# Kernel optimization log

Measured on AMD Instinct MI355X. Metric: run time of the kernel, lower is better.

## Reference

```python
import jax, jax.numpy as jnp
import numpy as np

D = 64          # node_hidden_dim
MP_STEPS = 6    # num_step_message_passing
S2S_STEPS = 6   # num_step_set2set
LSTM_LAYERS = 3 # num_layer_set2set


def setup_inputs() -> dict:
    key = jax.random.key(0)
    ks = jax.random.split(key, 32)
    N, E, B = 10000, 50000, 500
    node_in, edge_in, edge_hid, out_dim = 15, 5, 128, 12
    s = 0.1
    inp = {}
    inp["node_feat"] = jax.random.normal(ks[0], (N, node_in), jnp.float32)
    inp["edge_feat"] = jax.random.normal(ks[1], (E, edge_in), jnp.float32)
    inp["src"] = jax.random.randint(ks[2], (E,), 0, N)
    inp["dst"] = jax.random.randint(ks[3], (E,), 0, N)
    inp["graph_ids"] = jnp.sort(jax.random.randint(ks[4], (N,), 0, B))
    inp["num_graphs"] = B
    # lin0
    inp["lin0_W"] = jax.random.normal(ks[5], (node_in, D), jnp.float32) * s
    inp["lin0_b"] = jnp.zeros((D,), jnp.float32)
    # edge network MLP (Linear -> ReLU -> Linear), output reshaped to D x D per edge
    inp["em_W1"] = jax.random.normal(ks[6], (edge_in, edge_hid), jnp.float32) * s
    inp["em_b1"] = jnp.zeros((edge_hid,), jnp.float32)
    inp["em_W2"] = jax.random.normal(ks[7], (edge_hid, D * D), jnp.float32) * 0.02
    inp["em_b2"] = jnp.zeros((D * D,), jnp.float32)
    inp["conv_bias"] = jnp.zeros((D,), jnp.float32)
    # GRU (input D, hidden D), torch layout: [3*D, in], gate order r,z,n
    inp["gru_Wih"] = jax.random.normal(ks[8], (3 * D, D), jnp.float32) * s
    inp["gru_Whh"] = jax.random.normal(ks[9], (3 * D, D), jnp.float32) * s
    inp["gru_bih"] = jnp.zeros((3 * D,), jnp.float32)
    inp["gru_bhh"] = jnp.zeros((3 * D,), jnp.float32)
    # Set2Set LSTM: input 2*D, hidden D, 3 layers. torch layout [4*D, in], gates i,f,g,o
    inp["lstm0_Wih"] = jax.random.normal(ks[10], (4 * D, 2 * D), jnp.float32) * s
    inp["lstm0_Whh"] = jax.random.normal(ks[11], (4 * D, D), jnp.float32) * s
    inp["lstm0_bih"] = jnp.zeros((4 * D,), jnp.float32)
    inp["lstm0_bhh"] = jnp.zeros((4 * D,), jnp.float32)
    inp["lstm12_Wih"] = jax.random.normal(ks[12], (2, 4 * D, D), jnp.float32) * s
    inp["lstm12_Whh"] = jax.random.normal(ks[13], (2, 4 * D, D), jnp.float32) * s
    inp["lstm12_bih"] = jnp.zeros((2, 4 * D), jnp.float32)
    inp["lstm12_bhh"] = jnp.zeros((2, 4 * D), jnp.float32)
    # output head
    inp["lin1_W"] = jax.random.normal(ks[14], (2 * D, D), jnp.float32) * s
    inp["lin1_b"] = jnp.zeros((D,), jnp.float32)
    inp["lin2_W"] = jax.random.normal(ks[15], (D, out_dim), jnp.float32) * s
    inp["lin2_b"] = jnp.zeros((out_dim,), jnp.float32)
    return inp


def _mpnn(node_feat, edge_feat, src, dst, graph_ids, num_graphs,
          lin0_W, lin0_b, em_W1, em_b1, em_W2, em_b2, conv_bias,
          gru_Wih, gru_Whh, gru_bih, gru_bhh,
          lstm0_Wih, lstm0_Whh, lstm0_bih, lstm0_bhh,
          lstm12_Wih, lstm12_Whh, lstm12_bih, lstm12_bhh,
          lin1_W, lin1_b, lin2_W, lin2_b):
    N = node_feat.shape[0]
    E = edge_feat.shape[0]
    B = num_graphs
    # initial node embedding
    out = jax.nn.relu(node_feat @ lin0_W + lin0_b)      # [N, D]
    h = out                                             # GRU hidden (seq_len=1, 1 layer)
    # per-edge weight matrices (edge features are static across steps)
    We = (jax.nn.relu(edge_feat @ em_W1 + em_b1) @ em_W2 + em_b2).reshape(E, D, D)
    for _ in range(MP_STEPS):
        # NNConv: gather src -> per-edge matvec -> scatter-add to dst
        msg = jnp.einsum('ei,eio->eo', out[src], We)    # [E, D]
        agg = jax.ops.segment_sum(msg, dst, num_segments=N) + conv_bias
        m = jax.nn.relu(agg)                            # [N, D]
        # GRU cell (torch gate order r, z, n)
        gx = m @ gru_Wih.T + gru_bih
        gh = h @ gru_Whh.T + gru_bhh
        rx, zx, nx = jnp.split(gx, 3, axis=-1)
        rh, zh, nh = jnp.split(gh, 3, axis=-1)
        r = jax.nn.sigmoid(rx + rh)
        z = jax.nn.sigmoid(zx + zh)
        n = jnp.tanh(nx + r * nh)
        h = (1.0 - z) * n + z * h
        out = h
    # Set2Set readout: 3-layer LSTM over steps, attention over nodes per graph
    h_l = [jnp.zeros((B, D), out.dtype) for _ in range(LSTM_LAYERS)]
    c_l = [jnp.zeros((B, D), out.dtype) for _ in range(LSTM_LAYERS)]
    q_star = jnp.zeros((B, 2 * D), out.dtype)
    for _ in range(S2S_STEPS):
        x = q_star
        for l in range(LSTM_LAYERS):
            if l == 0:
                Wih, Whh, bih, bhh = lstm0_Wih, lstm0_Whh, lstm0_bih, lstm0_bhh
            else:
                Wih, Whh = lstm12_Wih[l - 1], lstm12_Whh[l - 1]
                bih, bhh = lstm12_bih[l - 1], lstm12_bhh[l - 1]
            g = x @ Wih.T + bih + h_l[l] @ Whh.T + bhh
            i_g, f_g, g_g, o_g = jnp.split(g, 4, axis=-1)
            c_l[l] = jax.nn.sigmoid(f_g) * c_l[l] + jax.nn.sigmoid(i_g) * jnp.tanh(g_g)
            h_l[l] = jax.nn.sigmoid(o_g) * jnp.tanh(c_l[l])
            x = h_l[l]
        q = x                                           # [B, D]
        # segment softmax attention
        e = jnp.sum(out * q[graph_ids], axis=-1)        # [N]
        emax = jax.ops.segment_max(e, graph_ids, num_segments=B)
        ex = jnp.exp(e - emax[graph_ids])
        denom = jax.ops.segment_sum(ex, graph_ids, num_segments=B)
        alpha = ex / denom[graph_ids]                   # [N]
        readout = jax.ops.segment_sum(alpha[:, None] * out, graph_ids, num_segments=B)
        q_star = jnp.concatenate([q, readout], axis=-1) # [B, 2D]
    y = jax.nn.relu(q_star @ lin1_W + lin1_b) @ lin2_W + lin2_b
    return y


def reference(node_feat, edge_feat, src, dst, graph_ids, num_graphs,
              lin0_W, lin0_b, em_W1, em_b1, em_W2, em_b2, conv_bias,
              gru_Wih, gru_Whh, gru_bih, gru_bhh,
              lstm0_Wih, lstm0_Whh, lstm0_bih, lstm0_bhh,
              lstm12_Wih, lstm12_Whh, lstm12_bih, lstm12_bhh,
              lin1_W, lin1_b, lin2_W, lin2_b):
    return _mpnn(node_feat, edge_feat, src, dst, graph_ids, num_graphs,
                 lin0_W, lin0_b, em_W1, em_b1, em_W2, em_b2, conv_bias,
                 gru_Wih, gru_Whh, gru_bih, gru_bhh,
                 lstm0_Wih, lstm0_Whh, lstm0_bih, lstm0_bhh,
                 lstm12_Wih, lstm12_Whh, lstm12_bih, lstm12_bhh,
                 lin1_W, lin1_b, lin2_W, lin2_b)
```

## Files before the change

### kernel.cpp

```cpp
#include <hip/hip_runtime.h>
#include <math.h>

#define NGRAPH 500
#define MP_STEPS 6
#define S2S_STEPS 6
#define S2S_CAP 64

typedef _Float16 h8 __attribute__((ext_vector_type(8)));
typedef float f4 __attribute__((ext_vector_type(4)));

__device__ __forceinline__ float sigmoidf_(float v){ return 1.0f/(1.0f + expf(-v)); }

__global__ void k_zero(float* __restrict__ p, int n){
  int i = blockIdx.x*256 + threadIdx.x;
  if(i < n) p[i] = 0.f;
}

__global__ void k_lin0(const float* __restrict__ nf, const float* __restrict__ W,
                       const float* __restrict__ b, const float* __restrict__ B2,
                       float* __restrict__ x, float* __restrict__ bm, int N){
  int n = blockIdx.x*4 + (threadIdx.x >> 6);
  int d = threadIdx.x & 63;
  if(n >= N) return;
  float acc = b[d];
#pragma unroll
  for(int i=0;i<15;i++) acc = fmaf(nf[n*15+i], W[i*64+d], acc);
  float xv = fmaxf(acc, 0.0f);
  x[n*64+d] = xv;
  float bmv = 0.f;
  for(int k=0;k<64;k++){
    float xk = __shfl(xv, k, 64);
    bmv = fmaf(xk, B2[k*64+d], bmv);
  }
  bm[(size_t)n*64+d] = bmv;
}

__global__ void k_edgeh(const float* __restrict__ ef, const float* __restrict__ W1,
                        const float* __restrict__ b1, _Float16* __restrict__ he, int E){
  int e = blockIdx.x*2 + (threadIdx.x >> 7);
  int h = threadIdx.x & 127;
  if(e >= E) return;
  float acc = b1[h];
#pragma unroll
  for(int i=0;i<5;i++) acc = fmaf(ef[e*5+i], W1[i*128+h], acc);
  he[(size_t)e*128 + h] = (_Float16)fmaxf(acc, 0.f);
}

__global__ void k_prepW2(const float* __restrict__ W2, _Float16* __restrict__ W2T){
  int idx = blockIdx.x*256 + threadIdx.x;
  if(idx >= 4096*128) return;
  int n = idx >> 7, k = idx & 127;
  W2T[idx] = (_Float16)W2[(size_t)k*4096 + n];
}

__global__ __launch_bounds__(256, 2) void k_fmsg(
    const _Float16* __restrict__ he,
    const _Float16* __restrict__ W2T,
    const float* __restrict__ x,
    const float* __restrict__ bm,
    const int* __restrict__ src, const int* __restrict__ dst,
    float* __restrict__ agg, int E)
{
  __shared__ _Float16 hs[128*128];
  __shared__ float xsT[64*132];
  __shared__ int ds_dst[128];
  __shared__ int ds_src[128];
  const int tid  = threadIdx.x;
  const int og   = tid >> 6;
  const int lane = tid & 63;
  const int quad = lane >> 4;
  const int l15  = lane & 15;
  const int e0   = blockIdx.x * 128;

  for(int t = tid; t < 2048; t += 256){
    int r = t >> 4, c = t & 15;
    uint4 v = make_uint4(0,0,0,0);
    if(e0 + r < E) v = *(const uint4*)&he[(size_t)(e0+r)*128 + c*8];
    *(uint4*)&hs[r*128 + c*8] = v;
  }
  {
    int j = tid >> 1, half = tid & 1;
    int sj = (e0 + j < E) ? src[e0 + j] : 0;
    const float4* xr = (const float4*)(x + (size_t)sj*64) + half*8;
#pragma unroll
    for(int k=0;k<8;k++){
      float4 v = xr[k];
      int ib = half*32 + k*4;
      xsT[(ib+0)*132 + j] = v.x;
      xsT[(ib+1)*132 + j] = v.y;
      xsT[(ib+2)*132 + j] = v.z;
      xsT[(ib+3)*132 + j] = v.w;
    }
  }
  if(tid < 128){
    ds_dst[tid] = (e0 + tid < E) ? dst[e0 + tid] : 0;
    ds_src[tid] = (e0 + tid < E) ? src[e0 + tid] : 0;
  }
  __syncthreads();

  h8 af[8][4];
#pragma unroll
  for(int mt=0;mt<8;mt++)
#pragma unroll
    for(int ks=0;ks<4;ks++)
      af[mt][ks] = *(const h8*)&hs[(mt*16 + l15)*128 + ks*32 + (quad<<3)];

  const _Float16* bbase = W2T + (size_t)(og*16 + l15)*128 + (quad<<3);

  f4 macc[8];
#pragma unroll
  for(int mt=0;mt<8;mt++) macc[mt] = (f4){0.f,0.f,0.f,0.f};

#pragma unroll 1
  for(int i=0;i<64;i++){
    const _Float16* bp = bbase + (size_t)i*64*128;
    h8 bf0 = *(const h8*)(bp);
    h8 bf1 = *(const h8*)(bp + 32);
    h8 bf2 = *(const h8*)(bp + 64);
    h8 bf3 = *(const h8*)(bp + 96);
    f4 g[8];
#pragma unroll
    for(int mt=0;mt<8;mt++) g[mt] = (f4){0.f,0.f,0.f,0.f};
#pragma unroll
    for(int mt=0;mt<8;mt++) g[mt] = __builtin_amdgcn_mfma_f32_16x16x32_f16(af[mt][0], bf0, g[mt], 0,0,0);
#pragma unroll
    for(int mt=0;mt<8;mt++) g[mt] = __builtin_amdgcn_mfma_f32_16x16x32_f16(af[mt][1], bf1, g[mt], 0,0,0);
#pragma unroll
    for(int mt=0;mt<8;mt++) g[mt] = __builtin_amdgcn_mfma_f32_16x16x32_f16(af[mt][2], bf2, g[mt], 0,0,0);
#pragma unroll
    for(int mt=0;mt<8;mt++) g[mt] = __builtin_amdgcn_mfma_f32_16x16x32_f16(af[mt][3], bf3, g[mt], 0,0,0);
#pragma unroll
    for(int mt=0;mt<8;mt++){
      f4 xf = *(const f4*)&xsT[i*132 + mt*16 + (quad<<2)];
      macc[mt] += xf * g[mt];
    }
  }

  const int col = og*16 + l15;
#pragma unroll
  for(int mt=0;mt<8;mt++){
#pragma unroll
    for(int r=0;r<4;r++){
      int edge = mt*16 + (quad<<2) + r;
      if(e0 + edge < E){
        float v = macc[mt][r] + bm[(size_t)ds_src[edge]*64 + col];
        atomicAdd(&agg[(size_t)ds_dst[edge]*64 + col], v);
      }
    }
  }
}

__global__ __launch_bounds__(256) void k_gru2(
    float* __restrict__ x, float* __restrict__ agg, const float* __restrict__ cb,
    const float* __restrict__ WihT, const float* __restrict__ WhhT,
    const float* __restrict__ bih, const float* __restrict__ bhh,
    const float* __restrict__ B2, float* __restrict__ bm, int N)
{
  __shared__ float ms[32*64], hs2[32*64];
  const int tid = threadIdx.x;
  const int n0 = blockIdx.x*32;
  for(int t=tid; t<2048; t+=256){
    int n = n0 + (t>>6), d = t&63;
    float mv=0.f, hv=0.f;
    if(n < N){
      mv = fmaxf(agg[(size_t)n*64+d] + cb[d], 0.f);
      agg[(size_t)n*64+d] = 0.f;
      hv = x[(size_t)n*64+d];
    }
    ms[t]=mv; hs2[t]=hv;
  }
  __syncthreads();
  const int gx = tid & 31, ng = tid >> 5;
  float ar[4][2]={{0}}, az[4][2]={{0}}, anx[4][2]={{0}}, anh[4][2]={{0}};
#pragma unroll 4
  for(int k=0;k<64;k++){
    float wi0=WihT[k*192+gx],     wi1=WihT[k*192+gx+32];
    float wi2=WihT[k*192+gx+64],  wi3=WihT[k*192+gx+96];
    float wi4=WihT[k*192+gx+128], wi5=WihT[k*192+gx+160];
    float wh0=WhhT[k*192+gx],     wh1=WhhT[k*192+gx+32];
    float wh2=WhhT[k*192+gx+64],  wh3=WhhT[k*192+gx+96];
    float wh4=WhhT[k*192+gx+128], wh5=WhhT[k*192+gx+160];
#pragma unroll
    for(int j=0;j<4;j++){
      float mk = ms[(ng*4+j)*64+k], hk = hs2[(ng*4+j)*64+k];
      ar[j][0] = fmaf(mk,wi0, fmaf(hk,wh0, ar[j][0]));
      ar[j][1] = fmaf(mk,wi1, fmaf(hk,wh1, ar[j][1]));
      az[j][0] = fmaf(mk,wi2, fmaf(hk,wh2, az[j][0]));
      az[j][1] = fmaf(mk,wi3, fmaf(hk,wh3, az[j][1]));
      anx[j][0]= fmaf(mk,wi4, anx[j][0]);
      anx[j][1]= fmaf(mk,wi5, anx[j][1]);
      anh[j][0]= fmaf(hk,wh4, anh[j][0]);
      anh[j][1]= fmaf(hk,wh5, anh[j][1]);
    }
  }
  float xn[4][2];
#pragma unroll
  for(int j=0;j<4;j++){
#pragma unroll
    for(int c=0;c<2;c++){
      int d = gx + 32*c;
      float r  = sigmoidf_(ar[j][c] + bih[d]     + bhh[d]);
      float z  = sigmoidf_(az[j][c] + bih[64+d]  + bhh[64+d]);
      float nn = tanhf(anx[j][c] + bih[128+d] + r*(anh[j][c] + bhh[128+d]));
      float hv = hs2[(ng*4+j)*64+d];
      xn[j][c] = (1.f - z)*nn + z*hv;
    }
  }
  __syncthreads();
#pragma unroll
  for(int j=0;j<4;j++){
#pragma unroll
    for(int c=0;c<2;c++){
      int n = n0 + ng*4 + j;
      ms[(ng*4+j)*64 + gx + 32*c] = xn[j][c];
      if(n < N) x[(size_t)n*64 + gx + 32*c] = xn[j][c];
    }
  }
  __syncthreads();
  float bmv[4][2] = {{0}};
#pragma unroll 4
  for(int d=0;d<64;d++){
    float b0 = B2[d*64+gx], b1 = B2[d*64+gx+32];
#pragma unroll
    for(int j=0;j<4;j++){
      float xd = ms[(ng*4+j)*64 + d];
      bmv[j][0] = fmaf(xd, b0, bmv[j][0]);
      bmv[j][1] = fmaf(xd, b1, bmv[j][1]);
    }
  }
#pragma unroll
  for(int j=0;j<4;j++){
    int n = n0 + ng*4 + j;
    if(n < N){
      bm[(size_t)n*64 + gx]      = bmv[j][0];
      bm[(size_t)n*64 + gx + 32] = bmv[j][1];
    }
  }
}

__global__ void k_tr_gru(const float* __restrict__ Wih, const float* __restrict__ Whh,
                         float* __restrict__ WihT, float* __restrict__ WhhT){
  int idx = blockIdx.x*256 + threadIdx.x;
  if(idx < 192*64){
    int r = idx/64, i = idx%64;
    WihT[i*192 + r] = Wih[idx];
    WhhT[i*192 + r] = Whh[idx];
  }
}

__device__ __forceinline__ int lbound(const int* __restrict__ a, int n, int v){
  int lo=0, hi=n;
  while(lo<hi){ int mid=(lo+hi)>>1; if(a[mid]<v) lo=mid+1; else hi=mid; }
  return lo;
}

template<int IN>
__device__ __forceinline__ void lstm_row(
    const float* __restrict__ xin, float* __restrict__ hv, float* __restrict__ cv,
    const float* __restrict__ Wih,
    const float* __restrict__ Whh,
    const float* __restrict__ bi, const float* __restrict__ bh,
    float* __restrict__ gs, int t)
{
  const float* wr = Wih + t*IN;
  const float* hr = Whh + t*64;
  float a0=0.f,a1=0.f,a2=0.f,a3=0.f;
#pragma unroll 8
  for(int k=0;k<IN;k+=4){
    f4 w = *(const f4*)&wr[k];
    f4 xv = *(const f4*)&xin[k];
    a0 = fmaf(w[0], xv[0], a0);
    a1 = fmaf(w[1], xv[1], a1);
    a2 = fmaf(w[2], xv[2], a2);
    a3 = fmaf(w[3], xv[3], a3);
  }
#pragma unroll 8
  for(int k=0;k<64;k+=4){
    f4 w = *(const f4*)&hr[k];
    f4 hvv = *(const f4*)&hv[k];
    a0 = fmaf(w[0], hvv[0], a0);
    a1 = fmaf(w[1], hvv[1], a1);
    a2 = fmaf(w[2], hvv[2], a2);
    a3 = fmaf(w[3], hvv[3], a3);
  }
  gs[t] = (a0+a1)+(a2+a3) + bi[t] + bh[t];
  __syncthreads();
  if(t < 64){
    float ig = sigmoidf_(gs[t]);
    float fg = sigmoidf_(gs[64+t]);
    float gg = tanhf(gs[128+t]);
    float og = sigmoidf_(gs[192+t]);
    float cn = fg*cv[t] + ig*gg;
    cv[t] = cn;
    hv[t] = og*tanhf(cn);
  }
  __syncthreads();
}

__global__ __launch_bounds__(256) void k_s2s(
    const float* __restrict__ x, const int* __restrict__ gid, int N,
    const float* __restrict__ l0_Wih, const float* __restrict__ l0_Whh,
    const float* __restrict__ l0_bih, const float* __restrict__ l0_bhh,
    const float* __restrict__ l12_Wih, const float* __restrict__ l12_Whh,
    const float* __restrict__ l12_bih, const float* __restrict__ l12_bhh,
    const float* __restrict__ W1, const float* __restrict__ b1,
    const float* __restrict__ W2, const float* __restrict__ b2,
    float* __restrict__ y)
{
  const int b = blockIdx.x;
  const int t = threadIdx.x;
  const int wave = t >> 6, lane = t & 63;
  __shared__ float xt[S2S_CAP*64];
  __shared__ float hsl[3][64], csl[3][64], qs[128], gs[256];
  __shared__ float ps[S2S_CAP], rop[4*64], wred[4], wsum[4];
  __shared__ int sh_n0, sh_n1;

  if(t == 0) sh_n0 = lbound(gid, N, b);
  if(t == 1) sh_n1 = lbound(gid, N, b+1);
  if(t < 192){ hsl[t>>6][t&63] = 0.f; csl[t>>6][t&63] = 0.f; }
  if(t < 128) qs[t] = 0.f;
  __syncthreads();
  const int n0 = sh_n0, cnt = sh_n1 - sh_n0;
  const int cc = (cnt < S2S_CAP) ? cnt : S2S_CAP;

  for(int j = wave; j < cc; j += 4)
    xt[j*64 + lane] = x[(size_t)(n0+j)*64 + lane];
  __syncthreads();

  for(int step=0; step<S2S_STEPS; step++){
    lstm_row<128>(qs,    hsl[0], csl[0], l0_Wih,            l0_Whh,            l0_bih,        l0_bhh,        gs, t);
    lstm_row<64>(hsl[0], hsl[1], csl[1], l12_Wih,           l12_Whh,           l12_bih,       l12_bhh,       gs, t);
    lstm_row<64>(hsl[1], hsl[2], csl[2], l12_Wih + 256*64,  l12_Whh + 256*64,  l12_bih + 256, l12_bhh + 256, gs, t);

    float qv = hsl[2][lane];
    float pm = -1e30f;
    for(int j = wave; j < cc; j += 4){
      float p = xt[j*64 + lane] * qv;
#pragma unroll
      for(int o=32;o;o>>=1) p += __shfl_xor(p, o, 64);
      if(lane == 0) ps[j] = p;
      pm = fmaxf(pm, p);
    }
    for(int j = S2S_CAP + wave; j < cnt; j += 4){
      float p = x[(size_t)(n0+j)*64 + lane] * qv;
#pragma unroll
      for(int o=32;o;o>>=1) p += __shfl_xor(p, o, 64);
      pm = fmaxf(pm, p);
    }
    if(lane == 0) wred[wave] = pm;
    __syncthreads();
    float mx = fmaxf(fmaxf(wred[0],wred[1]), fmaxf(wred[2],wred[3]));

    float pro = 0.f, pssum = 0.f;
    for(int j = wave; j < cc; j += 4){
      float ex = expf(ps[j] - mx);
      pssum += ex;
      pro = fmaf(ex, xt[j*64 + lane], pro);
    }
    for(int j = S2S_CAP + wave; j < cnt; j += 4){
      float xv = x[(size_t)(n0+j)*64 + lane];
      float p = xv * qv;
#pragma unroll
      for(int o=32;o;o>>=1) p += __shfl_xor(p, o, 64);
      float ex = expf(p - mx);
      pssum += ex;
      pro = fmaf(ex, xv, pro);
    }
    rop[wave*64 + lane] = pro;
    if(lane == 0) wsum[wave] = pssum;
    __syncthreads();
    if(t < 64){
      float tot = wsum[0]+wsum[1]+wsum[2]+wsum[3];
      float inv = (tot > 0.f) ? 1.f/tot : 0.f;
      float rv = (rop[t] + rop[64+t] + rop[128+t] + rop[192+t]) * inv;
      qs[t] = hsl[2][t];
      qs[64+t] = rv;
    }
    __syncthreads();
  }
  if(t < 64){
    float a = b1[t];
#pragma unroll 4
    for(int k=0;k<128;k++) a = fmaf(qs[k], W1[k*64+t], a);
    gs[t] = fmaxf(a, 0.f);
  }
  __syncthreads();
  if(t < 12){
    float o = b2[t];
#pragma unroll 4
    for(int k=0;k<64;k++) o = fmaf(gs[k], W2[k*12+t], o);
    y[b*12+t] = o;
  }
}

extern "C" void kernel_launch(void* const* d_in, const int* in_sizes, int n_in,
                              void* d_out, int out_size, void* d_ws, size_t ws_size,
                              hipStream_t stream) {
  const float* node_feat = (const float*)d_in[0];
  const float* edge_feat = (const float*)d_in[1];
  const int*   src       = (const int*)d_in[2];
  const int*   dst       = (const int*)d_in[3];
  const int*   gid       = (const int*)d_in[4];
  const float* lin0_W = (const float*)d_in[6];
  const float* lin0_b = (const float*)d_in[7];
  const float* em_W1  = (const float*)d_in[8];
  const float* em_b1  = (const float*)d_in[9];
  const float* em_W2  = (const float*)d_in[10];
  const float* em_b2  = (const float*)d_in[11];
  const float* conv_b = (const float*)d_in[12];
  const float* gru_Wih = (const float*)d_in[13];
  const float* gru_Whh = (const float*)d_in[14];
  const float* gru_bih = (const float*)d_in[15];
  const float* gru_bhh = (const float*)d_in[16];
  const float* l0_Wih = (const float*)d_in[17];
  const float* l0_Whh = (const float*)d_in[18];
  const float* l0_bih = (const float*)d_in[19];
  const float* l0_bhh = (const float*)d_in[20];
  const float* l12_Wih = (const float*)d_in[21];
  const float* l12_Whh = (const float*)d_in[22];
  const float* l12_bih = (const float*)d_in[23];
  const float* l12_bhh = (const float*)d_in[24];
  const float* lin1_W = (const float*)d_in[25];
  const float* lin1_b = (const float*)d_in[26];
  const float* lin2_W = (const float*)d_in[27];
  const float* lin2_b = (const float*)d_in[28];
  float* y = (float*)d_out;

  const int N = in_sizes[0] / 15;
  const int E = in_sizes[1] / 5;
  const int B = NGRAPH;

  char* p = (char*)d_ws;
  auto carve = [&](size_t bytes)->char* {
    char* r = p; p += (bytes + 255) & ~(size_t)255; return r;
  };
  _Float16* he_h = (_Float16*)carve((size_t)E*128*2);
  _Float16* W2T  = (_Float16*)carve((size_t)4096*128*2);
  float* x     = (float*)carve((size_t)N*64*4);
  float* agg   = (float*)carve((size_t)N*64*4);
  float* bmv   = (float*)carve((size_t)N*64*4);
  float* gWihT = (float*)carve(192*64*4);
  float* gWhhT = (float*)carve(192*64*4);
  (void)ws_size; (void)n_in; (void)out_size;

  k_lin0<<<(N+3)/4, 256, 0, stream>>>(node_feat, lin0_W, lin0_b, em_b2, x, bmv, N);
  k_edgeh<<<(E+1)/2, 256, 0, stream>>>(edge_feat, em_W1, em_b1, he_h, E);
  k_prepW2<<<(4096*128+255)/256, 256, 0, stream>>>(em_W2, W2T);
  k_tr_gru<<<(192*64+255)/256, 256, 0, stream>>>(gru_Wih, gru_Whh, gWihT, gWhhT);
  k_zero<<<(N*64+255)/256, 256, 0, stream>>>(agg, N*64);

  const int nblk = (E + 127) / 128;
  for(int s=0; s<MP_STEPS; s++){
    k_fmsg<<<nblk, 256, 0, stream>>>(he_h, W2T, x, bmv, src, dst, agg, E);
    k_gru2<<<(N+31)/32, 256, 0, stream>>>(x, agg, conv_b, gWihT, gWhhT,
                                          gru_bih, gru_bhh, em_b2, bmv, N);
  }

  k_s2s<<<B, 256, 0, stream>>>(x, gid, N,
                               l0_Wih, l0_Whh, l0_bih, l0_bhh,
                               l12_Wih, l12_Whh, l12_bih, l12_bhh,
                               lin1_W, lin1_b, lin2_W, lin2_b, y);
}
```

Measured before the change: 978.3 us.

## Double edge tile per block in message kernel and prefetch W2 fragments

Result: slower. 1.208 ms (+23.5%).

```diff
diff --git a/kernel.cpp b/kernel.cpp
--- a/kernel.cpp
+++ b/kernel.cpp
@@ -53,7 +53,7 @@
   W2T[idx] = (_Float16)W2[(size_t)k*4096 + n];
 }
 
-__global__ __launch_bounds__(256, 2) void k_fmsg(
+__global__ __launch_bounds__(256, 1) void k_fmsg(
     const _Float16* __restrict__ he,
     const _Float16* __restrict__ W2T,
     const float* __restrict__ x,
@@ -61,84 +61,85 @@
     const int* __restrict__ src, const int* __restrict__ dst,
     float* __restrict__ agg, int E)
 {
-  __shared__ _Float16 hs[128*128];
-  __shared__ float xsT[64*132];
-  __shared__ int ds_dst[128];
-  __shared__ int ds_src[128];
+  __shared__ _Float16 hs[256*128];
+  __shared__ float xsT[64*260];
+  __shared__ int ds_dst[256];
+  __shared__ int ds_src[256];
   const int tid  = threadIdx.x;
   const int og   = tid >> 6;
   const int lane = tid & 63;
   const int quad = lane >> 4;
   const int l15  = lane & 15;
-  const int e0   = blockIdx.x * 128;
-
-  for(int t = tid; t < 2048; t += 256){
+  const int e0   = blockIdx.x * 256;
+
+  for(int t = tid; t < 4096; t += 256){
     int r = t >> 4, c = t & 15;
     uint4 v = make_uint4(0,0,0,0);
     if(e0 + r < E) v = *(const uint4*)&he[(size_t)(e0+r)*128 + c*8];
     *(uint4*)&hs[r*128 + c*8] = v;
   }
   {
-    int j = tid >> 1, half = tid & 1;
+    int j = tid;
     int sj = (e0 + j < E) ? src[e0 + j] : 0;
-    const float4* xr = (const float4*)(x + (size_t)sj*64) + half*8;
-#pragma unroll
-    for(int k=0;k<8;k++){
+    const float4* xr = (const float4*)(x + (size_t)sj*64);
+#pragma unroll
+    for(int k=0;k<16;k++){
       float4 v = xr[k];
-      int ib = half*32 + k*4;
-      xsT[(ib+0)*132 + j] = v.x;
-      xsT[(ib+1)*132 + j] = v.y;
-      xsT[(ib+2)*132 + j] = v.z;
-      xsT[(ib+3)*132 + j] = v.w;
-    }
-  }
-  if(tid < 128){
-    ds_dst[tid] = (e0 + tid < E) ? dst[e0 + tid] : 0;
-    ds_src[tid] = (e0 + tid < E) ? src[e0 + tid] : 0;
-  }
-  __syncthreads();
-
-  h8 af[8][4];
-#pragma unroll
-  for(int mt=0;mt<8;mt++)
+      int ib = k*4;
+      xsT[(ib+0)*260 + j] = v.x;
+      xsT[(ib+1)*260 + j] = v.y;
+      xsT[(ib+2)*260 + j] = v.z;
+      xsT[(ib+3)*260 + j] = v.w;
+    }
+    ds_dst[j] = (e0 + j < E) ? dst[e0 + j] : 0;
+    ds_src[j] = sj;
+  }
+  __syncthreads();
+
+  h8 af[16][4];
+#pragma unroll
+  for(int mt=0;mt<16;mt++)
 #pragma unroll
     for(int ks=0;ks<4;ks++)
       af[mt][ks] = *(const h8*)&hs[(mt*16 + l15)*128 + ks*32 + (quad<<3)];
 
   const _Float16* bbase = W2T + (size_t)(og*16 + l15)*128 + (quad<<3);
 
-  f4 macc[8];
-#pragma unroll
-  for(int mt=0;mt<8;mt++) macc[mt] = (f4){0.f,0.f,0.f,0.f};
+  f4 macc[16];
+#pragma unroll
+  for(int mt=0;mt<16;mt++) macc[mt] = (f4){0.f,0.f,0.f,0.f};
+
+  h8 bf0 = *(const h8*)(bbase);
+  h8 bf1 = *(const h8*)(bbase + 32);
+  h8 bf2 = *(const h8*)(bbase + 64);
+  h8 bf3 = *(const h8*)(bbase + 96);
 
 #pragma unroll 1
   for(int i=0;i<64;i++){
-    const _Float16* bp = bbase + (size_t)i*64*128;
-    h8 bf0 = *(const h8*)(bp);
-    h8 bf1 = *(const h8*)(bp + 32);
-    h8 bf2 = *(const h8*)(bp + 64);
-    h8 bf3 = *(const h8*)(bp + 96);
-    f4 g[8];
-#pragma unroll
-    for(int mt=0;mt<8;mt++) g[mt] = (f4){0.f,0.f,0.f,0.f};
-#pragma unroll
-    for(int mt=0;mt<8;mt++) g[mt] = __builtin_amdgcn_mfma_f32_16x16x32_f16(af[mt][0], bf0, g[mt], 0,0,0);
-#pragma unroll
-    for(int mt=0;mt<8;mt++) g[mt] = __builtin_amdgcn_mfma_f32_16x16x32_f16(af[mt][1], bf1, g[mt], 0,0,0);
-#pragma unroll
-    for(int mt=0;mt<8;mt++) g[mt] = __builtin_amdgcn_mfma_f32_16x16x32_f16(af[mt][2], bf2, g[mt], 0,0,0);
-#pragma unroll
-    for(int mt=0;mt<8;mt++) g[mt] = __builtin_amdgcn_mfma_f32_16x16x32_f16(af[mt][3], bf3, g[mt], 0,0,0);
-#pragma unroll
-    for(int mt=0;mt<8;mt++){
-      f4 xf = *(const f4*)&xsT[i*132 + mt*16 + (quad<<2)];
-      macc[mt] += xf * g[mt];
-    }
+    h8 bn0, bn1, bn2, bn3;
+    if(i < 63){
+      const _Float16* np = bbase + (size_t)(i+1)*64*128;
+      bn0 = *(const h8*)(np);
+      bn1 = *(const h8*)(np + 32);
+      bn2 = *(const h8*)(np + 64);
+      bn3 = *(const h8*)(np + 96);
+    }
+#pragma unroll
+    for(int mt=0;mt<16;mt++){
+      f4 g = (f4){0.f,0.f,0.f,0.f};
+      g = __builtin_amdgcn_mfma_f32_16x16x32_f16(af[mt][0], bf0, g, 0,0,0);
+      g = __builtin_amdgcn_mfma_f32_16x16x32_f16(af[mt][1], bf1, g, 0,0,0);
+      g = __builtin_amdgcn_mfma_f32_16x16x32_f16(af[mt][2], bf2, g, 0,0,0);
+      g = __builtin_amdgcn_mfma_f32_16x16x32_f16(af[mt][3], bf3, g, 0,0,0);
+      f4 xf = *(const f4*)&xsT[i*260 + mt*16 + (quad<<2)];
+      macc[mt] += xf * g;
+    }
+    bf0 = bn0; bf1 = bn1; bf2 = bn2; bf3 = bn3;
   }
 
   const int col = og*16 + l15;
 #pragma unroll
-  for(int mt=0;mt<8;mt++){
+  for(int mt=0;mt<16;mt++){
 #pragma unroll
     for(int r=0;r<4;r++){
       int edge = mt*16 + (quad<<2) + r;
@@ -449,7 +450,7 @@
   k_tr_gru<<<(192*64+255)/256, 256, 0, stream>>>(gru_Wih, gru_Whh, gWihT, gWhhT);
   k_zero<<<(N*64+255)/256, 256, 0, stream>>>(agg, N*64);
 
-  const int nblk = (E + 127) / 128;
+  const int nblk = (E + 255) / 256;
   for(int s=0; s<MP_STEPS; s++){
     k_fmsg<<<nblk, 256, 0, stream>>>(he_h, W2T, x, bmv, src, dst, agg, E);
     k_gru2<<<(N+31)/32, 256, 0, stream>>>(x, agg, conv_b, gWihT, gWhhT,
```

## Precompute per-node transformed features and contract edge hidden states per source

Applied to the files above, without the earlier changes.

Result: slower. 2.486 ms (+154.1%).

```diff
diff --git a/kernel.cpp b/kernel.cpp
--- a/kernel.cpp
+++ b/kernel.cpp
@@ -7,6 +7,7 @@
 #define S2S_CAP 64
 
 typedef _Float16 h8 __attribute__((ext_vector_type(8)));
+typedef _Float16 h2 __attribute__((ext_vector_type(2)));
 typedef float f4 __attribute__((ext_vector_type(4)));
 
 __device__ __forceinline__ float sigmoidf_(float v){ return 1.0f/(1.0f + expf(-v)); }
@@ -53,11 +54,140 @@
   W2T[idx] = (_Float16)W2[(size_t)k*4096 + n];
 }
 
-__global__ __launch_bounds__(256, 2) void k_fmsg(
+__global__ void k_prepW2B(const float* __restrict__ W2, _Float16* __restrict__ W2B){
+  int idx = blockIdx.x*256 + threadIdx.x;
+  if(idx >= 128*64*64) return;
+  int k = idx >> 12, o = (idx >> 6) & 63, i = idx & 63;
+  W2B[idx] = (_Float16)W2[(size_t)k*4096 + i*64 + o];
+}
+
+__global__ void k_csr_count(const int* __restrict__ src, int* __restrict__ cnt, int E){
+  int e = blockIdx.x*256 + threadIdx.x;
+  if(e < E) atomicAdd(&cnt[src[e]], 1);
+}
+__global__ void k_scan(const int* __restrict__ cnt, int* __restrict__ rs, int N){
+  __shared__ int part[256];
+  int t = threadIdx.x;
+  int ch = (N + 255) / 256;
+  int s = 0;
+  for(int j=0;j<ch;j++){ int idx = t*ch+j; if(idx < N) s += cnt[idx]; }
+  part[t] = s;
+  __syncthreads();
+  if(t == 0){
+    int acc = 0;
+    for(int i=0;i<256;i++){ int v = part[i]; part[i] = acc; acc += v; }
+    rs[N] = acc;
+  }
+  __syncthreads();
+  int acc = part[t];
+  for(int j=0;j<ch;j++){
+    int idx = t*ch+j;
+    if(idx < N){ rs[idx] = acc; acc += cnt[idx]; }
+  }
+}
+__global__ void k_csr_scatter(const int* __restrict__ src, const int* __restrict__ rs,
+                              int* __restrict__ cur, int* __restrict__ eidx, int E){
+  int e = blockIdx.x*256 + threadIdx.x;
+  if(e < E){
+    int s = src[e];
+    int p = atomicAdd(&cur[s], 1);
+    eidx[rs[s] + p] = e;
+  }
+}
+
+__global__ __launch_bounds__(256, 2) void k_fmsgT(
     const _Float16* __restrict__ he,
-    const _Float16* __restrict__ W2T,
+    const _Float16* __restrict__ W2B,
     const float* __restrict__ x,
     const float* __restrict__ bm,
+    const int* __restrict__ src, const int* __restrict__ dst,
+    const int* __restrict__ rs, const int* __restrict__ eidx,
+    _Float16* __restrict__ T,
+    float* __restrict__ agg, int N, int E)
+{
+  __shared__ _Float16 xs[64*72];
+  __shared__ _Float16 heb[4][128];
+  const int tid  = threadIdx.x;
+  const int wave = tid >> 6;
+  const int lane = tid & 63;
+  const int quad = lane >> 4;
+  const int l15  = lane & 15;
+  const int n0   = blockIdx.x * 64;
+  _Float16* Tslab = T + (size_t)blockIdx.x * 64*128*64;
+
+  for(int t = tid; t < 4096; t += 256){
+    int n = t >> 6, i = t & 63;
+    float v = (n0 + n < N) ? x[(size_t)(n0+n)*64 + i] : 0.f;
+    xs[n*72 + i] = (_Float16)v;
+  }
+  __syncthreads();
+
+  h8 af[4][2];
+#pragma unroll
+  for(int mt=0;mt<4;mt++)
+#pragma unroll
+    for(int ks=0;ks<2;ks++)
+      af[mt][ks] = *(const h8*)&xs[(mt*16 + l15)*72 + ks*32 + (quad<<3)];
+
+  const int k0 = wave*32;
+  for(int k = k0; k < k0+32; k++){
+    const _Float16* wb = W2B + ((size_t)k << 12);
+    h8 bf[4][2];
+#pragma unroll
+    for(int ot=0;ot<4;ot++)
+#pragma unroll
+      for(int ks=0;ks<2;ks++)
+        bf[ot][ks] = *(const h8*)&wb[(ot*16 + l15)*64 + ks*32 + (quad<<3)];
+    f4 g[4][4];
+#pragma unroll
+    for(int mt=0;mt<4;mt++)
+#pragma unroll
+      for(int ot=0;ot<4;ot++){
+        f4 gg = (f4){0.f,0.f,0.f,0.f};
+        gg = __builtin_amdgcn_mfma_f32_16x16x32_f16(af[mt][0], bf[ot][0], gg, 0,0,0);
+        gg = __builtin_amdgcn_mfma_f32_16x16x32_f16(af[mt][1], bf[ot][1], gg, 0,0,0);
+        g[mt][ot] = gg;
+      }
+    const int kk = k >> 1, par = k & 1;
+#pragma unroll
+    for(int mt=0;mt<4;mt++)
+#pragma unroll
+      for(int ot=0;ot<4;ot++)
+#pragma unroll
+        for(int r=0;r<4;r++){
+          int node = mt*16 + (quad<<2) + r;
+          int o = ot*16 + l15;
+          Tslab[((node*64 + kk)<<7) + o*2 + par] = (_Float16)g[mt][ot][r];
+        }
+  }
+
+  __threadfence();
+  __syncthreads();
+
+  const int nend = (n0 + 64 < N) ? n0 + 64 : N;
+  const int es = rs[n0], ee = rs[nend];
+  for(int pos = es + wave; pos < ee; pos += 4){
+    int e = eidx[pos];
+    int s = src[e];
+    int d = dst[e];
+    int sl = s - n0;
+    *(uint*)&heb[wave][lane*2] = *(const uint*)&he[(size_t)e*128 + lane*2];
+    float acc = bm[(size_t)s*64 + lane];
+    const _Float16* Tr = Tslab + ((size_t)(sl*64) << 7) + lane*2;
+#pragma unroll 8
+    for(int kk=0; kk<64; kk++){
+      h2 tp = *(const h2*)(Tr + (kk<<7));
+      h2 hp = *(const h2*)&heb[wave][kk*2];
+      acc = fmaf((float)hp[0], (float)tp[0], acc);
+      acc = fmaf((float)hp[1], (float)tp[1], acc);
+    }
+    atomicAdd(&agg[(size_t)d*64 + lane], acc);
+  }
+}
+
+__global__ __launch_bounds__(256, 2) void k_fmsg(
+    const _Float16* __restrict__ he, const _Float16* __restrict__ W2T,
+    const float* __restrict__ x, const float* __restrict__ bm,
     const int* __restrict__ src, const int* __restrict__ dst,
     float* __restrict__ agg, int E)
 {
@@ -106,7 +236,6 @@
       af[mt][ks] = *(const h8*)&hs[(mt*16 + l15)*128 + ks*32 + (quad<<3)];
 
   const _Float16* bbase = W2T + (size_t)(og*16 + l15)*128 + (quad<<3);
-
   f4 macc[8];
 #pragma unroll
   for(int mt=0;mt<8;mt++) macc[mt] = (f4){0.f,0.f,0.f,0.f};
@@ -257,8 +386,7 @@
 template<int IN>
 __device__ __forceinline__ void lstm_row(
     const float* __restrict__ xin, float* __restrict__ hv, float* __restrict__ cv,
-    const float* __restrict__ Wih,
-    const float* __restrict__ Whh,
+    const float* __restrict__ Wih, const float* __restrict__ Whh,
     const float* __restrict__ bi, const float* __restrict__ bh,
     float* __restrict__ gs, int t)
 {
@@ -431,27 +559,50 @@
   const int B = NGRAPH;
 
   char* p = (char*)d_ws;
+  size_t used = 0;
   auto carve = [&](size_t bytes)->char* {
-    char* r = p; p += (bytes + 255) & ~(size_t)255; return r;
+    size_t a = (bytes + 255) & ~(size_t)255;
+    char* r = p + used; used += a; return r;
   };
   _Float16* he_h = (_Float16*)carve((size_t)E*128*2);
-  _Float16* W2T  = (_Float16*)carve((size_t)4096*128*2);
   float* x     = (float*)carve((size_t)N*64*4);
   float* agg   = (float*)carve((size_t)N*64*4);
   float* bmv   = (float*)carve((size_t)N*64*4);
   float* gWihT = (float*)carve(192*64*4);
   float* gWhhT = (float*)carve(192*64*4);
-  (void)ws_size; (void)n_in; (void)out_size;
+  _Float16* W2T = (_Float16*)carve((size_t)4096*128*2);
+  _Float16* W2B = (_Float16*)carve((size_t)128*64*64*2);
+  int* cnt  = (int*)carve((size_t)N*4);
+  int* rs   = (int*)carve((size_t)(N+1)*4);
+  int* eidx = (int*)carve((size_t)E*4);
+  const int nslab = (N + 63) / 64;
+  size_t tbytes = (size_t)nslab * 64 * 128 * 64 * 2;
+  bool use_T = (used + tbytes + 4096) <= ws_size;
+  _Float16* T = nullptr;
+  if(use_T) T = (_Float16*)carve(tbytes);
+  (void)n_in; (void)out_size;
 
   k_lin0<<<(N+3)/4, 256, 0, stream>>>(node_feat, lin0_W, lin0_b, em_b2, x, bmv, N);
   k_edgeh<<<(E+1)/2, 256, 0, stream>>>(edge_feat, em_W1, em_b1, he_h, E);
-  k_prepW2<<<(4096*128+255)/256, 256, 0, stream>>>(em_W2, W2T);
   k_tr_gru<<<(192*64+255)/256, 256, 0, stream>>>(gru_Wih, gru_Whh, gWihT, gWhhT);
   k_zero<<<(N*64+255)/256, 256, 0, stream>>>(agg, N*64);
-
-  const int nblk = (E + 127) / 128;
+  if(use_T){
+    k_prepW2B<<<(128*64*64+255)/256, 256, 0, stream>>>(em_W2, W2B);
+    k_zero<<<(N+255)/256, 256, 0, stream>>>((float*)cnt, N);
+    k_csr_count<<<(E+255)/256, 256, 0, stream>>>(src, cnt, E);
+    k_scan<<<1, 256, 0, stream>>>(cnt, rs, N);
+    k_zero<<<(N+255)/256, 256, 0, stream>>>((float*)cnt, N);
+    k_csr_scatter<<<(E+255)/256, 256, 0, stream>>>(src, rs, cnt, eidx, E);
+  } else {
+    k_prepW2<<<(4096*128+255)/256, 256, 0, stream>>>(em_W2, W2T);
+  }
+
   for(int s=0; s<MP_STEPS; s++){
-    k_fmsg<<<nblk, 256, 0, stream>>>(he_h, W2T, x, bmv, src, dst, agg, E);
+    if(use_T){
+      k_fmsgT<<<nslab, 256, 0, stream>>>(he_h, W2B, x, bmv, src, dst, rs, eidx, T, agg, N, E);
+    } else {
+      k_fmsg<<<(E+127)/128, 256, 0, stream>>>(he_h, W2T, x, bmv, src, dst, agg, E);
+    }
     k_gru2<<<(N+31)/32, 256, 0, stream>>>(x, agg, conv_b, gWihT, gWhhT,
                                           gru_bih, gru_bhh, em_b2, bmv, N);
   }
```
